# Performance work log

Hardware: AMD Instinct MI355X
Metric: run time of the kernel (lower is better)

The kernel has to match this reference:

```python
import jax, jax.numpy as jnp
import numpy as np

HIDDEN_DIM = 2048
NUM_HEADS = 16
HEAD_DIM = HIDDEN_DIM // NUM_HEADS


def setup_inputs() -> dict:
    key = jax.random.key(0)
    ks = jax.random.split(key, 5)
    B, S, D = 2, 2048, HIDDEN_DIM
    scale = 1.0 / np.sqrt(D)
    return {
        "x": jax.random.normal(ks[0], (B, S, D), dtype=jnp.float32),
        "w_q": jax.random.normal(ks[1], (D, D), dtype=jnp.float32) * scale,
        "w_k": jax.random.normal(ks[2], (D, D), dtype=jnp.float32) * scale,
        "w_v": jax.random.normal(ks[3], (D, D), dtype=jnp.float32) * scale,
        "w_o": jax.random.normal(ks[4], (D, D), dtype=jnp.float32) * scale,
        "causal": 1,
    }


def _attention(q, k, v, causal):
    # q,k,v: (B, S, D) -> split heads -> (B, H, S, d)
    B, S, D = q.shape
    q = q.reshape(B, S, NUM_HEADS, HEAD_DIM).transpose(0, 2, 1, 3)
    k = k.reshape(B, S, NUM_HEADS, HEAD_DIM).transpose(0, 2, 1, 3)
    v = v.reshape(B, S, NUM_HEADS, HEAD_DIM).transpose(0, 2, 1, 3)
    scale = 1.0 / np.sqrt(HEAD_DIM)
    # scores: (B, H, S, S)
    s = jnp.einsum("bhqd,bhkd->bhqk", q, k) * scale
    if causal:
        qpos = jnp.arange(S)[:, None]
        kpos = jnp.arange(S)[None, :]
        s = jnp.where(kpos > qpos, -jnp.inf, s)
    # stable softmax; rows that are fully -inf cannot occur with causal mask
    p = jax.nn.softmax(s, axis=-1)
    o = jnp.einsum("bhqk,bhkd->bhqd", p, v)
    return o.transpose(0, 2, 1, 3).reshape(B, S, D)


def reference(x, w_q, w_k, w_v, w_o, causal):
    q = x @ w_q.T
    k = x @ w_k.T
    v = x @ w_v.T
    o = _attention(q, k, v, bool(causal))
    return o @ w_o.T
```

## Files before the change

kernel.cpp:

```cpp
#include <hip/hip_runtime.h>


typedef __attribute__((ext_vector_type(8))) short short8;
typedef __attribute__((ext_vector_type(4))) short bfs4;
typedef __attribute__((ext_vector_type(4))) float floatx4;

__device__ __forceinline__ void gl_lds16(const void* g, void* l) {
  __builtin_amdgcn_global_load_lds((const __attribute__((address_space(1))) void*)g,
                                   (__attribute__((address_space(3))) void*)l, 16, 0, 0);
}

__device__ __forceinline__ short f2bf(float f) {
  union { float f; unsigned u; } a; a.f = f;
  unsigned r = a.u + 0x7FFFu + ((a.u >> 16) & 1u);
  return (short)(r >> 16);
}

__global__ __launch_bounds__(256) void cvt_bf16(
    const float* __restrict__ s0, const float* __restrict__ s1,
    const float* __restrict__ s2, const float* __restrict__ s3,
    const float* __restrict__ s4,
    short* __restrict__ d0, short* __restrict__ d1, short* __restrict__ d2,
    short* __restrict__ d3, short* __restrict__ d4,
    int n0, int nw) {
  const int z = blockIdx.z;
  const float* s = (z == 0) ? s0 : (z == 1) ? s1 : (z == 2) ? s2 : (z == 3) ? s3 : s4;
  short* d      = (z == 0) ? d0 : (z == 1) ? d1 : (z == 2) ? d2 : (z == 3) ? d3 : d4;
  const int n   = (z == 0) ? n0 : nw;
  const int stride = gridDim.x * blockDim.x * 4;
  for (int i = (blockIdx.x * blockDim.x + threadIdx.x) * 4; i < n; i += stride) {
    float4 v = *(const float4*)(s + i);
    bfs4 o;
    o[0] = f2bf(v.x); o[1] = f2bf(v.y); o[2] = f2bf(v.z); o[3] = f2bf(v.w);
    *(bfs4*)(d + i) = o;
  }
}

__global__ __launch_bounds__(256, 2) void gemm_bt(
    const short* __restrict__ A,
    const short* __restrict__ B0, const short* __restrict__ B1, const short* __restrict__ B2,
    short* __restrict__ C0, short* __restrict__ C1, short* __restrict__ C2,
    int M, int N, int K) {
  const short* Bm = (blockIdx.z == 0) ? B0 : ((blockIdx.z == 1) ? B1 : B2);
  short* C = (blockIdx.z == 0) ? C0 : ((blockIdx.z == 1) ? C1 : C2);

  __shared__ short As[128 * 64];
  __shared__ short Bs[128 * 64];

  const int tid = threadIdx.x;
  const int w = tid >> 6, l = tid & 63;
  const int lane15 = l & 15, quad = l >> 4;
  const int wr = w >> 1, wc = w & 1;
  const int row0 = blockIdx.y * 128;
  const int col0 = blockIdx.x * 128;

  floatx4 acc[4][4] = {};
  const int srow = l >> 3;
  const int sg = l & 7;

  for (int k0 = 0; k0 < K; k0 += 64) {
#pragma unroll
    for (int j = 0; j < 4; ++j) {
      int chunk = j * 4 + w;
      int row = chunk * 8 + srow;
      int g = sg ^ (row & 7);
      gl_lds16(A  + (size_t)(row0 + row) * K + k0 + g * 8, &As[chunk * 512]);
      gl_lds16(Bm + (size_t)(col0 + row) * K + k0 + g * 8, &Bs[chunk * 512]);
    }
    __syncthreads();
#pragma unroll
    for (int ks = 0; ks < 2; ++ks) {
      short8 af[4], bf[4];
#pragma unroll
      for (int i = 0; i < 4; ++i) {
        int rowA = wr * 64 + i * 16 + lane15;
        af[i] = *(const short8*)&As[rowA * 64 + (((ks * 4 + quad) ^ (rowA & 7)) << 3)];
        int rowB = wc * 64 + i * 16 + lane15;
        bf[i] = *(const short8*)&Bs[rowB * 64 + (((ks * 4 + quad) ^ (rowB & 7)) << 3)];
      }
#pragma unroll
      for (int i = 0; i < 4; ++i)
#pragma unroll
        for (int jj = 0; jj < 4; ++jj)
          acc[i][jj] = __builtin_amdgcn_mfma_f32_16x16x32_bf16(af[i], bf[jj], acc[i][jj], 0, 0, 0);
    }
    __syncthreads();
  }

#pragma unroll
  for (int i = 0; i < 4; ++i)
#pragma unroll
    for (int jj = 0; jj < 4; ++jj)
#pragma unroll
      for (int r = 0; r < 4; ++r) {
        int row = row0 + wr * 64 + i * 16 + quad * 4 + r;
        int col = col0 + wc * 64 + jj * 16 + lane15;
        C[(size_t)row * N + col] = f2bf(acc[i][jj][r]);
      }
}

__global__ __launch_bounds__(256, 2) void gemm_bt_f32out(
    const short* __restrict__ A, const short* __restrict__ Bm,
    float* __restrict__ C, int M, int N, int K) {
  __shared__ short As[128 * 64];
  __shared__ short Bs[128 * 64];

  const int tid = threadIdx.x;
  const int w = tid >> 6, l = tid & 63;
  const int lane15 = l & 15, quad = l >> 4;
  const int wr = w >> 1, wc = w & 1;
  const int row0 = blockIdx.y * 128;
  const int col0 = blockIdx.x * 128;

  floatx4 acc[4][4] = {};
  const int srow = l >> 3;
  const int sg = l & 7;

  for (int k0 = 0; k0 < K; k0 += 64) {
#pragma unroll
    for (int j = 0; j < 4; ++j) {
      int chunk = j * 4 + w;
      int row = chunk * 8 + srow;
      int g = sg ^ (row & 7);
      gl_lds16(A  + (size_t)(row0 + row) * K + k0 + g * 8, &As[chunk * 512]);
      gl_lds16(Bm + (size_t)(col0 + row) * K + k0 + g * 8, &Bs[chunk * 512]);
    }
    __syncthreads();
#pragma unroll
    for (int ks = 0; ks < 2; ++ks) {
      short8 af[4], bf[4];
#pragma unroll
      for (int i = 0; i < 4; ++i) {
        int rowA = wr * 64 + i * 16 + lane15;
        af[i] = *(const short8*)&As[rowA * 64 + (((ks * 4 + quad) ^ (rowA & 7)) << 3)];
        int rowB = wc * 64 + i * 16 + lane15;
        bf[i] = *(const short8*)&Bs[rowB * 64 + (((ks * 4 + quad) ^ (rowB & 7)) << 3)];
      }
#pragma unroll
      for (int i = 0; i < 4; ++i)
#pragma unroll
        for (int jj = 0; jj < 4; ++jj)
          acc[i][jj] = __builtin_amdgcn_mfma_f32_16x16x32_bf16(af[i], bf[jj], acc[i][jj], 0, 0, 0);
    }
    __syncthreads();
  }

#pragma unroll
  for (int i = 0; i < 4; ++i)
#pragma unroll
    for (int jj = 0; jj < 4; ++jj)
#pragma unroll
      for (int r = 0; r < 4; ++r) {
        int row = row0 + wr * 64 + i * 16 + quad * 4 + r;
        int col = col0 + wc * 64 + jj * 16 + lane15;
        C[(size_t)row * N + col] = acc[i][jj][r];
      }
}

__global__ __launch_bounds__(512, 4) void attn_fused(
    const short* __restrict__ Qg, const short* __restrict__ Kg,
    const short* __restrict__ Vg, short* __restrict__ Og,
    const int* __restrict__ causal_p) {
  constexpr int S = 2048, D = 2048, HDim = 128;
  constexpr int PS = 40;
  __shared__ __align__(16) short smem[38144];
  short* Ps  = smem + 32768;
  float* aLds = (float*)(smem + 37888);
  short* Qs  = smem;
  floatx4* F4 = (floatx4*)smem;

  const int tid = threadIdx.x;
  const int w = tid >> 6, l = tid & 63;
  const int lane15 = l & 15, quad = l >> 4;
  const int w4 = w & 3, grp = w >> 2;
  const int nlin = blockIdx.y * 16 + blockIdx.x;
  const int pairx = (nlin >> 3) & 15;
  const int bh = (nlin & 7) * 4 + (nlin >> 7);
  const int b = bh >> 4, h = bh & 15;
  const size_t rbase = (size_t)b * S;
  const int c0 = h * HDim;
  const int causal = *causal_p;
  short* Pw = Ps + w * (16 * PS);
  constexpr float SCL = 0.08838834764831845f * 1.4426950408889634f;

  const int krow = w * 4 + quad;
  const int kgs = lane15 ^ (krow & 7);
  const int vrow = l >> 1;
  const int vcol = w * 16 + (l & 1) * 8;

#pragma unroll 1
  for (int ph = 0; ph < 2; ++ph) {
    const int jt = ph ? (31 - pairx) : pairx;
    const int q0 = jt * 64;
    const int wrow0 = q0 + w4 * 16;

#pragma unroll
    for (int j = 0; j < 2; ++j) {
      int row = j * 32 + w * 4 + quad;
      int gs = lane15 ^ (row & 7);
      gl_lds16(Qg + (rbase + q0 + row) * D + c0 + gs * 8, &Qs[(j * 8 + w) * 512]);
    }
    __syncthreads();
    short8 qf[4];
#pragma unroll
    for (int ks = 0; ks < 4; ++ks) {
      int row = w4 * 16 + lane15;
      qf[ks] = *(const short8*)&Qs[row * HDim + (((ks * 4 + quad) ^ (row & 7)) << 3)];
    }
    __syncthreads();

    floatx4 ot[8] = {};
    float psum[4] = {0.f, 0.f, 0.f, 0.f};
    const int ktiles = causal ? (q0 / 32 + 2) : (S / 32);
    const int iters = ktiles >> 1;

    short* Kcur = smem;
    short* Knxt = smem + 8192;
    short* Vcur = smem + 16384;
    short* Vnxt = smem + 24576;

    gl_lds16(Kg + (rbase + krow) * D + c0 + kgs * 8, &Kcur[w * 512]);
    gl_lds16(Kg + (rbase + 32 + krow) * D + c0 + kgs * 8, &Kcur[4096 + w * 512]);
    gl_lds16(Vg + (rbase + vrow) * D + c0 + vcol, &Vcur[w * 512]);
    gl_lds16(Vg + (rbase + 32 + vrow) * D + c0 + vcol, &Vcur[4096 + w * 512]);
    __syncthreads();

    for (int it = 0; it < iters; ++it) {
      const int k0A = it * 64;
      const bool pf = (it + 1 < iters);
      if (pf) {
        const int k0N = k0A + 64;
        gl_lds16(Kg + (rbase + k0N + krow) * D + c0 + kgs * 8, &Knxt[w * 512]);
        gl_lds16(Kg + (rbase + k0N + 32 + krow) * D + c0 + kgs * 8, &Knxt[4096 + w * 512]);
        gl_lds16(Vg + (rbase + k0N + vrow) * D + c0 + vcol, &Vnxt[w * 512]);
        gl_lds16(Vg + (rbase + k0N + 32 + vrow) * D + c0 + vcol, &Vnxt[4096 + w * 512]);
      }

      const int k0 = k0A + grp * 32;
      const short* Kc = Kcur + grp * 4096;
      const short* Vc = Vcur + grp * 4096;
      if (!causal || k0 <= wrow0 + 15) {
        floatx4 sacc[2] = {};
#pragma unroll
        for (int ks = 0; ks < 4; ++ks) {
          short8 kf0, kf1;
          {
            int row = lane15;
            kf0 = *(const short8*)&Kc[row * HDim + (((ks * 4 + quad) ^ (row & 7)) << 3)];
            row = 16 + lane15;
            kf1 = *(const short8*)&Kc[row * HDim + (((ks * 4 + quad) ^ (row & 7)) << 3)];
          }
          sacc[0] = __builtin_amdgcn_mfma_f32_16x16x32_bf16(qf[ks], kf0, sacc[0], 0, 0, 0);
          sacc[1] = __builtin_amdgcn_mfma_f32_16x16x32_bf16(qf[ks], kf1, sacc[1], 0, 0, 0);
        }
#pragma unroll
        for (int r = 0; r < 4; ++r) {
          int prow = quad * 4 + r;
          int qrow = wrow0 + prow;
          float s0 = fminf(sacc[0][r] * SCL, 115.0f);
          float s1 = fminf(sacc[1][r] * SCL, 115.0f);
          float p0 = exp2f(s0);
          float p1 = exp2f(s1);
          if (causal) {
            if (k0 + lane15 > qrow)      p0 = 0.f;
            if (k0 + 16 + lane15 > qrow) p1 = 0.f;
          }
          psum[r] += p0 + p1;
          Pw[prow * PS + lane15]      = f2bf(p0);
          Pw[prow * PS + 16 + lane15] = f2bf(p1);
        }
        short8 pfr = *(const short8*)&Pw[lane15 * PS + quad * 8];
        const unsigned vbase = (unsigned)(size_t)Vc + (quad << 8) + (lane15 << 3);
        bfs4 vlo[8], vhi[8];
#pragma unroll
        for (int cd = 0; cd < 8; ++cd)
          asm volatile("ds_read_b64_tr_b16 %0, %2\n\t"
                       "ds_read_b64_tr_b16 %1, %2 offset:128"
                       : "=&v"(vlo[cd]), "=&v"(vhi[cd])
                       : "v"(vbase + (cd << 10)));
        asm volatile("s_waitcnt lgkmcnt(0)" ::: "memory");
        __builtin_amdgcn_sched_barrier(0);
#pragma unroll
        for (int cd = 0; cd < 8; ++cd) {
          short8 vf = {vlo[cd][0], vlo[cd][1], vlo[cd][2], vlo[cd][3],
                       vhi[cd][0], vhi[cd][1], vhi[cd][2], vhi[cd][3]};
          ot[cd] = __builtin_amdgcn_mfma_f32_16x16x32_bf16(vf, pfr, ot[cd], 0, 0, 0);
        }
      }

      __syncthreads();
      short* t = Kcur; Kcur = Knxt; Knxt = t;
      t = Vcur; Vcur = Vnxt; Vnxt = t;
    }

#pragma unroll
    for (int r = 0; r < 4; ++r) {
      float s = psum[r];
      s += __shfl_xor(s, 1, 64);
      s += __shfl_xor(s, 2, 64);
      s += __shfl_xor(s, 4, 64);
      s += __shfl_xor(s, 8, 64);
      if (lane15 == 0) aLds[grp * 64 + w4 * 16 + quad * 4 + r] = s;
    }
    if (grp == 1) {
      int qrow = w4 * 16 + lane15;
#pragma unroll
      for (int cd = 0; cd < 8; ++cd)
        F4[qrow * 32 + ((cd * 4 + quad) ^ ((qrow & 7) << 2))] = ot[cd];
    }
    __syncthreads();
    float invq = 0.f;
    if (grp == 0) {
      int qrow = w4 * 16 + lane15;
      invq = 1.0f / (aLds[qrow] + aLds[64 + qrow]);
#pragma unroll
      for (int cd = 0; cd < 8; ++cd) {
        floatx4 o2 = F4[qrow * 32 + ((cd * 4 + quad) ^ ((qrow & 7) << 2))];
        ot[cd] += o2;
      }
    }
    __syncthreads();
    if (grp == 0) {
      int qrow = w4 * 16 + lane15;
#pragma unroll
      for (int cd = 0; cd < 8; ++cd)
#pragma unroll
        for (int r = 0; r < 4; ++r) {
          int col = cd * 16 + quad * 4 + r;
          Qs[qrow * HDim + (((col >> 3) ^ (qrow & 7)) << 3) + (col & 7)] =
              f2bf(ot[cd][r] * invq);
        }
    }
    __syncthreads();
#pragma unroll
    for (int i = 0; i < 2; ++i) {
      int c = i * 512 + tid;
      int row = c >> 4, g = c & 15;
      *(short8*)(Og + (rbase + q0 + row) * D + c0 + g * 8) =
          *(const short8*)&Qs[row * HDim + ((g ^ (row & 7)) << 3)];
    }
    __syncthreads();
  }
}

extern "C" void kernel_launch(void* const* d_in, const int* in_sizes, int n_in,
                              void* d_out, int out_size, void* d_ws, size_t ws_size,
                              hipStream_t stream) {
  const float* x  = (const float*)d_in[0];
  const float* wq = (const float*)d_in[1];
  const float* wk = (const float*)d_in[2];
  const float* wv = (const float*)d_in[3];
  const float* wo = (const float*)d_in[4];
  const int* causal = (const int*)d_in[5];
  float* out = (float*)d_out;

  const int M = 4096, N = 2048, K = 2048;
  const int NX = M * K;
  const int NW = N * K;

  char* ws = (char*)d_ws;
  short* xb  = (short*)(ws);
  short* wqb = (short*)(ws + 16u * 1024 * 1024);
  short* wkb = (short*)(ws + 24u * 1024 * 1024);
  short* wvb = (short*)(ws + 32u * 1024 * 1024);
  short* wob = (short*)(ws + 40u * 1024 * 1024);
  short* q   = (short*)(ws + 48u * 1024 * 1024);
  short* k   = (short*)(ws + 64u * 1024 * 1024);
  short* v   = (short*)(ws + 80u * 1024 * 1024);
  short* o   = (short*)(ws + 96u * 1024 * 1024);

  dim3 blk(256);
  cvt_bf16<<<dim3(2048, 1, 5), blk, 0, stream>>>(x, wq, wk, wv, wo,
                                                 xb, wqb, wkb, wvb, wob, NX, NW);
  gemm_bt<<<dim3(N / 128, M / 128, 3), blk, 0, stream>>>(xb, wqb, wkb, wvb,
                                                         q, k, v, M, N, K);
  attn_fused<<<dim3(16, 32), dim3(512), 0, stream>>>(q, k, v, o, causal);
  gemm_bt_f32out<<<dim3(N / 128, M / 128, 1), blk, 0, stream>>>(o, wob, out, M, N, K);
}
```

Measured before the change: 377.2 us.

## Fuse Q/K/V projections into one block sharing the A tile

Each GEMM block now computes the Q, K and V output tiles together, loading the x tile into LDS once and reusing it against three weight tiles. This removes the separate z-dimension launches and the triplicated reads of x. In exchange it triples the accumulator registers and grows LDS use per block, which risks spills or lower occupancy and leaves fewer blocks to spread across CUs.

```diff
diff --git a/kernel.cpp b/kernel.cpp
--- a/kernel.cpp
+++ b/kernel.cpp
@@ -41,11 +41,8 @@
     const short* __restrict__ B0, const short* __restrict__ B1, const short* __restrict__ B2,
     short* __restrict__ C0, short* __restrict__ C1, short* __restrict__ C2,
     int M, int N, int K) {
-  const short* Bm = (blockIdx.z == 0) ? B0 : ((blockIdx.z == 1) ? B1 : B2);
-  short* C = (blockIdx.z == 0) ? C0 : ((blockIdx.z == 1) ? C1 : C2);
-
   __shared__ short As[128 * 64];
-  __shared__ short Bs[128 * 64];
+  __shared__ short Bs[3][128 * 64];
 
   const int tid = threadIdx.x;
   const int w = tid >> 6, l = tid & 63;
@@ -54,7 +51,9 @@
   const int row0 = blockIdx.y * 128;
   const int col0 = blockIdx.x * 128;
 
-  floatx4 acc[4][4] = {};
+  floatx4 acc0[4][4] = {};
+  floatx4 acc1[4][4] = {};
+  floatx4 acc2[4][4] = {};
   const int srow = l >> 3;
   const int sg = l & 7;
 
@@ -65,24 +64,58 @@
       int row = chunk * 8 + srow;
       int g = sg ^ (row & 7);
       gl_lds16(A  + (size_t)(row0 + row) * K + k0 + g * 8, &As[chunk * 512]);
-      gl_lds16(Bm + (size_t)(col0 + row) * K + k0 + g * 8, &Bs[chunk * 512]);
+      gl_lds16(B0 + (size_t)(col0 + row) * K + k0 + g * 8, &Bs[0][chunk * 512]);
+      gl_lds16(B1 + (size_t)(col0 + row) * K + k0 + g * 8, &Bs[1][chunk * 512]);
+      gl_lds16(B2 + (size_t)(col0 + row) * K + k0 + g * 8, &Bs[2][chunk * 512]);
     }
     __syncthreads();
 #pragma unroll
     for (int ks = 0; ks < 2; ++ks) {
-      short8 af[4], bf[4];
+      short8 af[4];
 #pragma unroll
       for (int i = 0; i < 4; ++i) {
         int rowA = wr * 64 + i * 16 + lane15;
         af[i] = *(const short8*)&As[rowA * 64 + (((ks * 4 + quad) ^ (rowA & 7)) << 3)];
-        int rowB = wc * 64 + i * 16 + lane15;
-        bf[i] = *(const short8*)&Bs[rowB * 64 + (((ks * 4 + quad) ^ (rowB & 7)) << 3)];
-      }
-#pragma unroll
-      for (int i = 0; i < 4; ++i)
-#pragma unroll
-        for (int jj = 0; jj < 4; ++jj)
-          acc[i][jj] = __builtin_amdgcn_mfma_f32_16x16x32_bf16(af[i], bf[jj], acc[i][jj], 0, 0, 0);
+      }
+      {
+        short8 bf[4];
+#pragma unroll
+        for (int i = 0; i < 4; ++i) {
+          int rowB = wc * 64 + i * 16 + lane15;
+          bf[i] = *(const short8*)&Bs[0][rowB * 64 + (((ks * 4 + quad) ^ (rowB & 7)) << 3)];
+        }
+#pragma unroll
+        for (int i = 0; i < 4; ++i)
+#pragma unroll
+          for (int jj = 0; jj < 4; ++jj)
+            acc0[i][jj] = __builtin_amdgcn_mfma_f32_16x16x32_bf16(af[i], bf[jj], acc0[i][jj], 0, 0, 0);
+      }
+      {
+        short8 bf[4];
+#pragma unroll
+        for (int i = 0; i < 4; ++i) {
+          int rowB = wc * 64 + i * 16 + lane15;
+          bf[i] = *(const short8*)&Bs[1][rowB * 64 + (((ks * 4 + quad) ^ (rowB & 7)) << 3)];
+        }
+#pragma unroll
+        for (int i = 0; i < 4; ++i)
+#pragma unroll
+          for (int jj = 0; jj < 4; ++jj)
+            acc1[i][jj] = __builtin_amdgcn_mfma_f32_16x16x32_bf16(af[i], bf[jj], acc1[i][jj], 0, 0, 0);
+      }
+      {
+        short8 bf[4];
+#pragma unroll
+        for (int i = 0; i < 4; ++i) {
+          int rowB = wc * 64 + i * 16 + lane15;
+          bf[i] = *(const short8*)&Bs[2][rowB * 64 + (((ks * 4 + quad) ^ (rowB & 7)) << 3)];
+        }
+#pragma unroll
+        for (int i = 0; i < 4; ++i)
+#pragma unroll
+          for (int jj = 0; jj < 4; ++jj)
+            acc2[i][jj] = __builtin_amdgcn_mfma_f32_16x16x32_bf16(af[i], bf[jj], acc2[i][jj], 0, 0, 0);
+      }
     }
     __syncthreads();
   }
@@ -95,7 +128,9 @@
       for (int r = 0; r < 4; ++r) {
         int row = row0 + wr * 64 + i * 16 + quad * 4 + r;
         int col = col0 + wc * 64 + jj * 16 + lane15;
-        C[(size_t)row * N + col] = f2bf(acc[i][jj][r]);
+        C0[(size_t)row * N + col] = f2bf(acc0[i][jj][r]);
+        C1[(size_t)row * N + col] = f2bf(acc1[i][jj][r]);
+        C2[(size_t)row * N + col] = f2bf(acc2[i][jj][r]);
       }
 }
 
@@ -372,8 +407,8 @@
   dim3 blk(256);
   cvt_bf16<<<dim3(2048, 1, 5), blk, 0, stream>>>(x, wq, wk, wv, wo,
                                                  xb, wqb, wkb, wvb, wob, NX, NW);
-  gemm_bt<<<dim3(N / 128, M / 128, 3), blk, 0, stream>>>(xb, wqb, wkb, wvb,
-                                                         q, k, v, M, N, K);
+  gemm_bt<<<dim3(N / 128, M / 128), blk, 0, stream>>>(xb, wqb, wkb, wvb,
+                                                      q, k, v, M, N, K);
   attn_fused<<<dim3(16, 32), dim3(512), 0, stream>>>(q, k, v, o, causal);
   gemm_bt_f32out<<<dim3(N / 128, M / 128, 1), blk, 0, stream>>>(o, wob, out, M, N, K);
 }
```

New measurement: 381.0 us. No clear change (+1.0%).
